# Kernel optimization log

Hardware: AMD Instinct MI355X
Metric: run time of the kernel (lower is better)

Reference implementation:

```python
import jax, jax.numpy as jnp
import numpy as np

WL = 140        # window_length
TD_NUM = 14     # TimeDelayEnd - TimeDelaySta = 21 - 7
OFC = 119       # window_length - TimeDelayEnd
E1 = 119        # td_attn embed dim
E2 = 16         # cm_attn embed dim


def _mha(q, k, v, in_w, in_b, out_w, out_b):
    # single-head MultiheadAttention, torch convention: y = x @ W.T + b
    E = q.shape[-1]
    qp = q @ in_w[:E].T + in_b[:E]
    kp = k @ in_w[E:2 * E].T + in_b[E:2 * E]
    vp = v @ in_w[2 * E:].T + in_b[2 * E:]
    attn = jax.nn.softmax((qp * (E ** -0.5)) @ kp.T, axis=-1)
    return (attn @ vp) @ out_w.T + out_b


def setup_inputs() -> dict:
    key = jax.random.key(0)
    ks = jax.random.split(key, 24)
    n = lambda i, s: jax.random.normal(ks[i], s, dtype=jnp.float32) * 0.05
    return {
        "x": jax.random.normal(ks[0], (1, 1, 18, WL), dtype=jnp.float32),
        "td_in_w": n(1, (3 * E1, E1)), "td_in_b": n(2, (3 * E1,)),
        "td_out_w": n(3, (E1, E1)), "td_out_b": n(4, (E1,)),
        "cm_in_w": n(5, (4, 3 * E2, E2)), "cm_in_b": n(6, (4, 3 * E2)),
        "cm_out_w": n(7, (4, E2, E2)), "cm_out_b": n(8, (4, E2)),
        "mc_w": n(9, (2, 16)), "mc_b": n(10, (2,)),
        "max_fc_w": n(11, (16, 32)), "max_fc_b": n(12, (16,)),
        "proj_w": n(13, (2, 16)),
        "ln_g": jnp.ones((16,), jnp.float32), "ln_b": jnp.zeros((16,), jnp.float32),
        "fc_w": n(14, (2,)), "fc_b": n(15, (2,)),
        "out1_w": n(16, (OFC, 2 * OFC)), "out1_b": n(17, (OFC,)),
        "out2_w": n(18, (2, OFC)), "out2_b": n(19, (2,)),
    }


def reference(x, td_in_w, td_in_b, td_out_w, td_out_b,
              cm_in_w, cm_in_b, cm_out_w, cm_out_b,
              mc_w, mc_b, max_fc_w, max_fc_b, proj_w,
              ln_g, ln_b, fc_w, fc_b, out1_w, out1_b, out2_w, out2_b):
    wavA = x[0, 0, 0]            # [140]
    eeg = x[0, 0, 1:17]          # [16, 140]
    wavB = x[0, 0, 17]           # [140]

    # ChannelWav: vectorized sliding-window gather -> [OFC, TD_NUM]
    idx = jnp.arange(OFC)[:, None] + jnp.arange(TD_NUM)[None, :]
    wA_win = wavA[idx]           # [119, 14]
    wB_win = wavB[idx]

    eeg_q = eeg[:, WL - OFC:]    # [16, 119] (16 eeg channels as seq, embed=119)

    # time-delay attention: query=eeg (len 16), key/value=delayed wav (len 14)
    wA_att = _mha(eeg_q, wA_win.T, wA_win.T, td_in_w, td_in_b, td_out_w, td_out_b)  # [16,119]
    wB_att = _mha(eeg_q, wB_win.T, wB_win.T, td_in_w, td_in_b, td_out_w, td_out_b)

    # select_max: bmm + 1x1 conv + relu + fc + argmax over 16 scores
    vA = jax.nn.relu(mc_w[0] @ (eeg_q @ wA_att.T) + mc_b[0])   # [16]
    vB = jax.nn.relu(mc_w[1] @ (eeg_q @ wB_att.T) + mc_b[1])
    weight = jax.nn.relu(max_fc_w @ jnp.concatenate([vA, vB]) + max_fc_b)
    mi = jnp.argmax(weight)     # note: clamped into [0, TD_NUM) by jnp.take
    wA_sel = jnp.take(wA_win.T, mi, axis=0)   # [119]
    wB_sel = jnp.take(wB_win.T, mi, axis=0)

    # proj_audio: Conv1d(1,16,1,bias=False) == outer product with weight vector
    wA_p = proj_w[0][:, None] * wA_sel[None, :]   # [16,119]
    wB_p = proj_w[1][:, None] * wB_sel[None, :]

    # LayerNorm over the 16-channel axis
    et = eeg_q.T                                   # [119,16]
    mu = et.mean(-1, keepdims=True)
    var = et.var(-1, keepdims=True)
    eeg_ln = (((et - mu) / jnp.sqrt(var + 1e-5)) * ln_g + ln_b).T   # [16,119]

    data = [wA_p, eeg_ln, eeg_ln, wB_p]
    kv = [eeg_ln, wA_p, wB_p, eeg_ln]
    outs = [_mha(data[i].T, kv[i].T, kv[i].T,
                 cm_in_w[i], cm_in_b[i], cm_out_w[i], cm_out_b[i]).T
            for i in range(4)]                      # each [16,119]

    # tensordot + diag == per-position channel dot product
    d0 = jnp.einsum('ct,ct->t', outs[0], outs[1])   # [119]
    d1 = jnp.einsum('ct,ct->t', outs[3], outs[2])
    s0 = jax.nn.sigmoid(fc_w[0] * d0 + fc_b[0])
    s1 = jax.nn.sigmoid(fc_w[1] * d1 + fc_b[1])
    dd = jnp.concatenate([s0, s1])                  # [238]

    h = jax.nn.sigmoid(out1_w @ dd + out1_b)
    return jax.nn.sigmoid(out2_w @ h + out2_b)[None, :]   # [1,2]
```

## Files before the change

### kernel.cpp

```cpp
#include <hip/hip_runtime.h>
#include <math.h>


#define NWG 8
#define NT  1024

constexpr int WLEN = 140;
constexpr int TDN  = 14;
constexpr int NOFC = 119;

constexpr int G_V16 = 0;
constexpr int G_DD  = 64;

constexpr int EEG = 0;
constexpr int WA  = 1904;
constexpr int WB  = 2044;
constexpr int LNT = 2184;
constexpr int QP4 = 4088;
constexpr int Z4  = 4564;
constexpr int UD  = 5040;
constexpr int WTT = 5160;
constexpr int WVV = 5280;
constexpr int VT  = 5400;
constexpr int SC4 = 5416;
constexpr int BKQ = 5472;
constexpr int CVB = 5476, CBO = 5477;
constexpr int WQH = 5480;
constexpr int WKL = 5496;
constexpr int WVL = 5512;
constexpr int WQT = 5528;
constexpr int CST = 5544;
constexpr int AC  = 5548;
constexpr int BC  = 5564;
constexpr int G1L = 5580;
constexpr int MXT = 5612;
constexpr int MXB = 6124;
constexpr int KPH = 6144;
constexpr int VPS = 8048;
constexpr int S1H = 10428;
constexpr int S2H = 10547;
constexpr int OWS = 10668;
constexpr int OBS = 10924;
constexpr int O1W = 10944;
constexpr int O1B = 14544;
constexpr int O2WS= 14560;
constexpr int O2B = 14590;
constexpr int FCW = 14592;
constexpr int FCB = 14594;
constexpr int DDL = 14596;
constexpr int HHL = 14836;
constexpr int VSL = 14852;
constexpr int ARENA = 14884;

struct Args {
  const float *x, *td_in_w, *td_in_b, *td_out_w, *td_out_b;
  const float *cm_in_w, *cm_in_b, *cm_out_w, *cm_out_b;
  const float *mc_w, *mc_b, *max_fc_w, *max_fc_b, *proj_w;
  const float *ln_g, *ln_b, *fc_w, *fc_b;
  const float *out1_w, *out1_b, *out2_w, *out2_b;
  float *out;
  unsigned int *bar;
  float *G;
};

__device__ __forceinline__ float sigmf(float v) {
  return 1.0f / (1.0f + __expf(-v));
}

__device__ __forceinline__ void gbar(unsigned int* p) {
  __syncthreads();
  if (threadIdx.x == 0) {
    __hip_atomic_fetch_add(p, 1u, __ATOMIC_ACQ_REL, __HIP_MEMORY_SCOPE_AGENT);
    while (__hip_atomic_load(p, __ATOMIC_RELAXED, __HIP_MEMORY_SCOPE_AGENT) < (unsigned)NWG) {
      __builtin_amdgcn_s_sleep(1);
    }
    __builtin_amdgcn_fence(__ATOMIC_ACQUIRE, "agent");
  }
  __syncthreads();
}

__device__ __forceinline__ float dot119(const float* __restrict__ w,
                                        const float* __restrict__ x,
                                        int lane16) {
  float a0 = 0.f, a1 = 0.f;
#pragma unroll
  for (int t = 0; t < 7; ++t) {
    float wv = w[lane16 + 16 * t];
    float xv = x[lane16 + 16 * t];
    if (t & 1) a1 += wv * xv; else a0 += wv * xv;
  }
  if (lane16 < 7) a0 += w[112 + lane16] * x[112 + lane16];
  float acc = a0 + a1;
#pragma unroll
  for (int m = 1; m < 16; m <<= 1) acc += __shfl_xor(acc, m);
  return acc;
}

__device__ __forceinline__ float dot16f4(const float* __restrict__ x,
                                         const float* __restrict__ w) {
  const float4* xa = (const float4*)x; const float4* wa = (const float4*)w;
  float4 x0 = xa[0], x1 = xa[1], x2 = xa[2], x3 = xa[3];
  float4 w0 = wa[0], w1 = wa[1], w2 = wa[2], w3 = wa[3];
  float d0 = x0.x*w0.x + x0.y*w0.y + x0.z*w0.z + x0.w*w0.w;
  float d1 = x1.x*w1.x + x1.y*w1.y + x1.z*w1.z + x1.w*w1.w;
  float d2 = x2.x*w2.x + x2.y*w2.y + x2.z*w2.z + x2.w*w2.w;
  float d3 = x3.x*w3.x + x3.y*w3.y + x3.z*w3.z + x3.w*w3.w;
  return (d0 + d1) + (d2 + d3);
}

__global__ __launch_bounds__(NT) void fused_cnn_kernel(Args a) {
  __shared__ __align__(16) float S[ARENA];
  const int tid = threadIdx.x;
  const int wgid = blockIdx.x;
  const int grp = tid >> 4;
  const int lane16 = tid & 15;
  float* G = a.G;

  const int s  = wgid >> 2;
  const int i0 = (wgid & 3) * 4;
  const int mh = s ? 3 : 0;
  const int lm = s ? 2 : 1;
  const int q4 = wgid & 3;
  const int r0 = q4 * 30;
  const int nr = (q4 == 3) ? 29 : 30;
  const int wavX = s ? WB : WA;

  for (int t = tid; t < 16 * NOFC; t += NT) {
    int c = t / NOFC, tt = t - c * NOFC;
    S[EEG + t] = a.x[(1 + c) * WLEN + (WLEN - NOFC) + tt];
  }
  if (tid < WLEN) {
    S[WA + tid] = a.x[tid];
    S[WB + tid] = a.x[17 * WLEN + tid];
  }
  if (tid < 512) {
    int t16 = tid >> 5, c32 = tid & 31;
    S[MXT + c32 * 16 + t16] = a.max_fc_w[tid];
  }
  if (tid < 16)  S[MXB + tid] = a.max_fc_b[tid];
  for (int idx = tid; idx < 15 * 238; idx += NT) {
    int rl = idx / 238, c = idx - rl * 238;
    int r = wgid * 15 + rl;
    S[O1W + rl * 240 + c] = (r < NOFC) ? a.out1_w[r * 238 + c] : 0.0f;
  }
  if (tid < 15) {
    int r = wgid * 15 + tid;
    S[O1B + tid] = (r < NOFC) ? a.out1_b[r] : 0.0f;
  }
  if (tid < 30) {
    int o = tid / 15, j = tid - o * 15;
    int r = wgid * 15 + j;
    S[O2WS + tid] = (r < NOFC) ? a.out2_w[o * NOFC + r] : 0.0f;
  }
  if (tid < 2) {
    S[O2B + tid] = a.out2_b[tid];
    S[FCW + tid] = a.fc_w[tid];
    S[FCB + tid] = a.fc_b[tid];
  }
  __syncthreads();

  for (int e = grp; e < NOFC; e += 64) {
    const float* wrow = a.td_in_w + e * NOFC;
    float w0 = wrow[lane16], w1 = wrow[lane16 + 16], w2 = wrow[lane16 + 32],
          w3 = wrow[lane16 + 48], w4 = wrow[lane16 + 64], w5 = wrow[lane16 + 80],
          w6 = wrow[lane16 + 96];
    float wt7 = (lane16 < 7) ? wrow[112 + lane16] : 0.0f;
    float b = a.td_in_b[e];
#pragma unroll
    for (int kk = 0; kk < 4; ++kk) {
      const float* x = S + EEG + (i0 + kk) * NOFC;
      float acc = w0 * x[lane16] + w1 * x[lane16 + 16] + w2 * x[lane16 + 32]
                + w3 * x[lane16 + 48] + w4 * x[lane16 + 64] + w5 * x[lane16 + 80]
                + w6 * x[lane16 + 96];
      if (lane16 < 7) acc += wt7 * x[112 + lane16];
#pragma unroll
      for (int mm = 1; mm < 16; mm <<= 1) acc += __shfl_xor(acc, mm);
      if (lane16 == 0) S[QP4 + kk * NOFC + e] = acc + b;
    }
  }
  if (grp >= 55) {
    int d = (grp - 55) * 16 + lane16;
    if (d < NOFC) {
      float acc = 0.f;
#pragma unroll
      for (int i = 0; i < 16; ++i) acc += a.mc_w[s * 16 + i] * S[EEG + i * NOFC + d];
      S[UD + d] = acc;
    }
  }
  __syncthreads();

  if (tid < NOFC) {
    float xv[16]; float mu = 0.f;
#pragma unroll
    for (int c = 0; c < 16; ++c) { xv[c] = S[EEG + c * NOFC + tid]; mu += xv[c]; }
    mu *= (1.0f / 16.0f);
    float var = 0.f;
#pragma unroll
    for (int c = 0; c < 16; ++c) { float d = xv[c] - mu; var += d * d; }
    var *= (1.0f / 16.0f);
    float inv = 1.0f / sqrtf(var + 1e-5f);
#pragma unroll
    for (int c = 0; c < 16; ++c)
      S[LNT + tid * 16 + c] = (xv[c] - mu) * inv * a.ln_g[c] + a.ln_b[c];
  } else if (tid >= 128 && tid < 128 + NOFC) {
    int t = tid - 128;
    float a0 = 0.f, a1 = 0.f, a2 = 0.f, a3 = 0.f;
    for (int e = 0; e < NOFC; ++e) {
      float w = a.td_in_w[(NOFC + e) * NOFC + t];
      a0 += S[QP4 + e] * w;
      a1 += S[QP4 + NOFC + e] * w;
      a2 += S[QP4 + 2 * NOFC + e] * w;
      a3 += S[QP4 + 3 * NOFC + e] * w;
    }
    S[Z4 + t] = a0; S[Z4 + NOFC + t] = a1;
    S[Z4 + 2 * NOFC + t] = a2; S[Z4 + 3 * NOFC + t] = a3;
  } else if (tid >= 256 && tid < 320) {
    int kk = (tid - 256) >> 4;
    float acc = dot119(S + QP4 + kk * NOFC, a.td_in_b + NOFC, lane16);
    if (lane16 == 0) S[BKQ + kk] = acc;
  } else if (tid >= 320 && tid < 320 + NOFC) {
    int t = tid - 320;
    float acc = 0.f;
    for (int d = 0; d < NOFC; ++d) acc += S[UD + d] * a.td_out_w[d * NOFC + t];
    S[WTT + t] = acc;
  } else if (tid >= 448 && tid < 464) {
    int e = tid - 448;
    float acc = 0.f;
#pragma unroll
    for (int c = 0; c < 16; ++c) acc += a.proj_w[s * 16 + c] * a.cm_in_w[(mh * 48 + e) * 16 + c];
    S[WQH + e] = acc;
  } else if (tid >= 464 && tid < 480) {
    int e = tid - 464;
    float acc = 0.f;
#pragma unroll
    for (int c = 0; c < 16; ++c) acc += a.proj_w[s * 16 + c] * a.cm_in_w[(lm * 48 + 16 + e) * 16 + c];
    S[WKL + e] = acc;
  } else if (tid >= 480 && tid < 496) {
    int e = tid - 480;
    float acc = 0.f;
#pragma unroll
    for (int c = 0; c < 16; ++c) acc += a.proj_w[s * 16 + c] * a.cm_in_w[(lm * 48 + 32 + e) * 16 + c];
    S[WVL + e] = acc;
  }
  if (grp >= 36) {
#pragma unroll
    for (int rnd = 0; rnd < 2; ++rnd) {
      int idx = (grp - 36) + rnd * 28;
      if (idx < 56) {
        int kk = idx / TDN, j = idx - kk * TDN;
        float acc = dot119(S + wavX + j, S + Z4 + kk * NOFC, lane16);
        if (lane16 == 0)
          S[SC4 + kk * TDN + j] = 0.09166984970282113f * (acc + S[BKQ + kk]);
      }
    }
  }
  __syncthreads();

  if (tid < NOFC) {
    float acc = 0.f;
    for (int e = 0; e < NOFC; ++e) acc += S[WTT + e] * a.td_in_w[(2 * NOFC + e) * NOFC + tid];
    S[WVV + tid] = acc;
  } else if (tid >= 120 && tid < 124) {
    int k = tid - 120;
    float* r = S + SC4 + k * TDN;
    float mx = r[0];
#pragma unroll
    for (int j = 1; j < TDN; ++j) mx = fmaxf(mx, r[j]);
    float sum = 0.f;
#pragma unroll
    for (int j = 0; j < TDN; ++j) { float p = __expf(r[j] - mx); r[j] = p; sum += p; }
    float inv = 1.0f / sum;
#pragma unroll
    for (int j = 0; j < TDN; ++j) r[j] *= inv;
  } else if (tid >= 128 && tid < 144) {
    int c = tid - 128;
    float acc = 0.f;
#pragma unroll
    for (int e = 0; e < 16; ++e) acc += a.cm_in_w[(lm * 48 + e) * 16 + c] * S[WKL + e];
    S[WQT + c] = acc;
  } else if (tid == 144) {
    float acc = 0.f;
#pragma unroll
    for (int e = 0; e < 16; ++e) acc += a.cm_in_b[lm * 48 + e] * S[WKL + e];
    S[CST] = acc;
  } else if (tid >= 160 && tid < 176) {
    int c = tid - 160;
    float acc = 0.f;
#pragma unroll
    for (int e = 0; e < 16; ++e) acc += a.cm_out_w[lm * 256 + c * 16 + e] * S[WVL + e];
    S[AC + c] = acc;
  } else if (tid >= 176 && tid < 192) {
    int c = tid - 176;
    float acc = 0.f;
#pragma unroll
    for (int e = 0; e < 16; ++e) acc += a.cm_out_w[lm * 256 + c * 16 + e] * a.cm_in_b[lm * 48 + 32 + e];
    S[BC + c] = acc + a.cm_out_b[lm * 16 + c];
  } else if (tid == 192) {
    float acc = 0.f;
    for (int e = 0; e < NOFC; ++e) acc += a.td_in_b[2 * NOFC + e] * S[WTT + e];
    S[CVB] = acc;
  } else if (tid == 193) {
    float acc = 0.f;
    for (int d = 0; d < NOFC; ++d) acc += S[UD + d] * a.td_out_b[d];
    S[CBO] = acc;
  }
  if (tid >= 256) {
    for (int o = tid - 256; o < 4080; o += 768) {
      if (o < 1904) {
        int u = o >> 4, e = o & 15;
        S[KPH + o] = dot16f4(S + LNT + u * 16, a.cm_in_w + (mh * 48 + 16 + e) * 16)
                     + a.cm_in_b[mh * 48 + 16 + e];
      } else if (o < 3808) {
        int o2 = o - 1904, u = o2 >> 4, e = o2 & 15;
        S[VPS + u * 20 + e] = dot16f4(S + LNT + u * 16, a.cm_in_w + (mh * 48 + 32 + e) * 16)
                              + a.cm_in_b[mh * 48 + 32 + e];
      } else if (o < 4064) {
        int o2 = o - 3808, c = o2 >> 4, e = o2 & 15;
        S[OWS + e * 16 + c] = a.cm_out_w[mh * 256 + o2];
      } else {
        S[OBS + o - 4064] = a.cm_out_b[mh * 16 + (o - 4064)];
      }
    }
  }
  __syncthreads();

  if (grp < TDN) {
    float acc = dot119(S + wavX + grp, S + WVV, lane16);
    if (lane16 == 0) S[VT + grp] = acc;
  }
  if (tid >= 256 && tid < 256 + 30) {
    int rl = tid - 256;
    if (rl < nr) {
      int t = r0 + rl;
      float acc = S[CST];
#pragma unroll
      for (int c = 0; c < 16; ++c) acc += S[LNT + t * 16 + c] * S[WQT + c];
      S[G1L + rl] = acc;
    }
  }
  if (tid >= 512 && tid < 512 + 238) {
    int idx = tid - 512;
    int u = (idx < NOFC) ? idx : idx - NOFC;
    const float* kpr = S + KPH + u * 16;
    float acc = 0.f;
    if (idx < NOFC) {
#pragma unroll
      for (int e = 0; e < 16; ++e) acc += S[WQH + e] * kpr[e];
      S[S1H + u] = acc;
    } else {
#pragma unroll
      for (int e = 0; e < 16; ++e) acc += a.cm_in_b[mh * 48 + e] * kpr[e];
      S[S2H + u] = acc;
    }
  }
  __syncthreads();

  if (tid < 4) {
    float acc = 0.f;
#pragma unroll
    for (int j = 0; j < TDN; ++j) acc += S[SC4 + tid * TDN + j] * S[VT + j];
    float v = acc + S[CVB] + S[CBO] + a.mc_b[s];
    G[G_V16 + s * 16 + i0 + tid] = fmaxf(v, 0.f);
  }
  gbar(a.bar + 0);

  if (tid < 32) S[VSL + tid] = G[G_V16 + tid];
  __syncthreads();
  int mi;
  {
    float wl = S[MXB + lane16];
#pragma unroll
    for (int c = 0; c < 32; ++c) wl += S[MXT + c * 16 + lane16] * S[VSL + c];
    wl = fmaxf(wl, 0.f);
    float mx = wl;
#pragma unroll
    for (int d = 1; d < 16; d <<= 1) mx = fmaxf(mx, __shfl_xor(mx, d));
    int cand = (wl == mx) ? lane16 : 99;
#pragma unroll
    for (int d = 1; d < 16; d <<= 1) cand = min(cand, __shfl_xor(cand, d));
    mi = min(cand, TDN - 1);
  }

  if (grp < nr) {
    const int t = r0 + grp;
    const float wselq = S[wavX + t + mi];
    float p[8];
    float sum = 0.f;
#pragma unroll
    for (int cc = 0; cc < 8; ++cc) {
      int u = lane16 + cc * 16;
      float e1 = 0.f;
      if (u < NOFC)
        e1 = __expf(0.25f * (wselq * S[S1H + u] + S[S2H + u]));
      p[cc] = e1;
      sum += e1;
    }
#pragma unroll
    for (int d = 1; d < 16; d <<= 1) sum += __shfl_xor(sum, d);
    float inv = 1.0f / sum;

    float oa[16];
#pragma unroll
    for (int e = 0; e < 16; ++e) oa[e] = 0.f;
#pragma unroll
    for (int cc = 0; cc < 8; ++cc) {
      int u = lane16 + cc * 16;
      if (u < NOFC) {
        const float4* v4 = (const float4*)(S + VPS + u * 20);
        float4 v0 = v4[0], v1 = v4[1], v2 = v4[2], v3 = v4[3];
        float pv = p[cc];
        oa[0] += pv*v0.x; oa[1] += pv*v0.y; oa[2] += pv*v0.z; oa[3] += pv*v0.w;
        oa[4] += pv*v1.x; oa[5] += pv*v1.y; oa[6] += pv*v1.z; oa[7] += pv*v1.w;
        oa[8] += pv*v2.x; oa[9] += pv*v2.y; oa[10] += pv*v2.z; oa[11] += pv*v2.w;
        oa[12] += pv*v3.x; oa[13] += pv*v3.y; oa[14] += pv*v3.z; oa[15] += pv*v3.w;
      }
    }
#pragma unroll
    for (int e = 0; e < 16; ++e) {
#pragma unroll
      for (int d = 1; d < 16; d <<= 1) oa[e] += __shfl_xor(oa[e], d);
    }
    float oc = S[OBS + lane16];
#pragma unroll
    for (int e = 0; e < 16; ++e) oc += oa[e] * inv * S[OWS + e * 16 + lane16];
    float dA = oc * S[AC + lane16];
    float dB = oc * S[BC + lane16];
#pragma unroll
    for (int d = 1; d < 16; d <<= 1) {
      dA += __shfl_xor(dA, d);
      dB += __shfl_xor(dB, d);
    }
    const float g = S[G1L + grp];
    float s0 = 0.f, s1a = 0.f;
#pragma unroll
    for (int cc = 0; cc < 8; ++cc) {
      int u = lane16 + cc * 16;
      if (u < NOFC) {
        float w = S[wavX + u + mi];
        float e1 = __expf(0.25f * g * w);
        s0 += e1; s1a += e1 * w;
      }
    }
#pragma unroll
    for (int d = 1; d < 16; d <<= 1) {
      s0 += __shfl_xor(s0, d);
      s1a += __shfl_xor(s1a, d);
    }
    float h = s1a / s0;
    float dval = h * dA + dB;
    if (lane16 == 0)
      G[G_DD + s * NOFC + t] = sigmf(S[FCW + s] * dval + S[FCB + s]);
  }
  gbar(a.bar + 16);

  if (tid < 238) S[DDL + tid] = G[G_DD + tid];
  __syncthreads();
  if (grp < 15) {
    int r = wgid * 15 + grp;
    float acc = 0.f;
#pragma unroll
    for (int k = 0; k < 15; ++k) {
      int c = lane16 + 16 * k;
      if (c < 238) acc += S[O1W + grp * 240 + c] * S[DDL + c];
    }
#pragma unroll
    for (int d = 1; d < 16; d <<= 1) acc += __shfl_xor(acc, d);
    if (lane16 == 0)
      S[HHL + grp] = (r < NOFC) ? sigmf(acc + S[O1B + grp]) : 0.0f;
  }
  __syncthreads();
  if (tid == 0) {
    float p0 = 0.f, p1 = 0.f;
#pragma unroll
    for (int j = 0; j < 15; ++j) {
      p0 += S[O2WS + j] * S[HHL + j];
      p1 += S[O2WS + 15 + j] * S[HHL + j];
    }
    float* acc = (float*)((char*)a.bar + 128);
    unsigned int* done = (unsigned int*)((char*)a.bar + 192);
    __hip_atomic_fetch_add(acc + 0, p0, __ATOMIC_RELAXED, __HIP_MEMORY_SCOPE_AGENT);
    __hip_atomic_fetch_add(acc + 1, p1, __ATOMIC_RELAXED, __HIP_MEMORY_SCOPE_AGENT);
    unsigned old = __hip_atomic_fetch_add(done, 1u, __ATOMIC_ACQ_REL, __HIP_MEMORY_SCOPE_AGENT);
    if (old == NWG - 1) {
      __builtin_amdgcn_fence(__ATOMIC_ACQUIRE, "agent");
      float a0 = __hip_atomic_load(acc + 0, __ATOMIC_RELAXED, __HIP_MEMORY_SCOPE_AGENT);
      float a1 = __hip_atomic_load(acc + 1, __ATOMIC_RELAXED, __HIP_MEMORY_SCOPE_AGENT);
      a.out[0] = sigmf(a0 + S[O2B + 0]);
      a.out[1] = sigmf(a1 + S[O2B + 1]);
    }
  }
}

extern "C" void kernel_launch(void* const* d_in, const int* in_sizes, int n_in,
                              void* d_out, int out_size, void* d_ws, size_t ws_size,
                              hipStream_t stream) {
  Args a;
  a.x        = (const float*)d_in[0];
  a.td_in_w  = (const float*)d_in[1];
  a.td_in_b  = (const float*)d_in[2];
  a.td_out_w = (const float*)d_in[3];
  a.td_out_b = (const float*)d_in[4];
  a.cm_in_w  = (const float*)d_in[5];
  a.cm_in_b  = (const float*)d_in[6];
  a.cm_out_w = (const float*)d_in[7];
  a.cm_out_b = (const float*)d_in[8];
  a.mc_w     = (const float*)d_in[9];
  a.mc_b     = (const float*)d_in[10];
  a.max_fc_w = (const float*)d_in[11];
  a.max_fc_b = (const float*)d_in[12];
  a.proj_w   = (const float*)d_in[13];
  a.ln_g     = (const float*)d_in[14];
  a.ln_b     = (const float*)d_in[15];
  a.fc_w     = (const float*)d_in[16];
  a.fc_b     = (const float*)d_in[17];
  a.out1_w   = (const float*)d_in[18];
  a.out1_b   = (const float*)d_in[19];
  a.out2_w   = (const float*)d_in[20];
  a.out2_b   = (const float*)d_in[21];
  a.out      = (float*)d_out;
  a.bar      = (unsigned int*)d_ws;
  a.G        = (float*)((char*)d_ws + 512);

  hipMemsetAsync(d_ws, 0, 512, stream);
  fused_cnn_kernel<<<dim3(NWG), dim3(NT), 0, stream>>>(a);
}
```

Baseline: 34.66 us.

## Remove final grid barrier via atomic partial out1 sums and split-K td matvecs

```diff
diff --git a/kernel.cpp b/kernel.cpp
--- a/kernel.cpp
+++ b/kernel.cpp
@@ -10,47 +10,47 @@
 constexpr int NOFC = 119;
 
 constexpr int G_V16 = 0;
-constexpr int G_DD  = 64;
 
 constexpr int EEG = 0;
 constexpr int WA  = 1904;
 constexpr int WB  = 2044;
 constexpr int LNT = 2184;
 constexpr int QP4 = 4088;
-constexpr int Z4  = 4564;
-constexpr int UD  = 5040;
-constexpr int WTT = 5160;
-constexpr int WVV = 5280;
-constexpr int VT  = 5400;
-constexpr int SC4 = 5416;
-constexpr int BKQ = 5472;
-constexpr int CVB = 5476, CBO = 5477;
-constexpr int WQH = 5480;
-constexpr int WKL = 5496;
-constexpr int WVL = 5512;
-constexpr int WQT = 5528;
-constexpr int CST = 5544;
-constexpr int AC  = 5548;
-constexpr int BC  = 5564;
-constexpr int G1L = 5580;
-constexpr int MXT = 5612;
-constexpr int MXB = 6124;
-constexpr int KPH = 6144;
-constexpr int VPS = 8048;
-constexpr int S1H = 10428;
-constexpr int S2H = 10547;
-constexpr int OWS = 10668;
-constexpr int OBS = 10924;
-constexpr int O1W = 10944;
-constexpr int O1B = 14544;
-constexpr int O2WS= 14560;
-constexpr int O2B = 14590;
-constexpr int FCW = 14592;
-constexpr int FCB = 14594;
-constexpr int DDL = 14596;
-constexpr int HHL = 14836;
-constexpr int VSL = 14852;
-constexpr int ARENA = 14884;
+constexpr int Z8  = 4564;
+constexpr int UD  = 5516;
+constexpr int WT2 = 5636;
+constexpr int WV2 = 5876;
+constexpr int VT  = 6114;
+constexpr int SC4 = 6128;
+constexpr int BKQ = 6184;
+constexpr int CVB = 6188, CBO = 6189;
+constexpr int WQH = 6192;
+constexpr int WKL = 6208;
+constexpr int WVL = 6224;
+constexpr int WQT = 6240;
+constexpr int CST = 6256;
+constexpr int AC  = 6260;
+constexpr int BC  = 6276;
+constexpr int G1L = 6292;
+constexpr int MXT = 6324;
+constexpr int MXB = 6836;
+constexpr int KPH = 6852;
+constexpr int VPS = 8756;
+constexpr int S1H = 11136;
+constexpr int S2H = 11255;
+constexpr int OWS = 11376;
+constexpr int OBS = 11632;
+constexpr int O1C = 11648;
+constexpr int O1B = 15340;
+constexpr int O2WS= 15460;
+constexpr int O2B = 15698;
+constexpr int FCW = 15700;
+constexpr int FCB = 15702;
+constexpr int DD30= 15704;
+constexpr int HH  = 15736;
+constexpr int VSL = 15856;
+constexpr int FLG = 15888;
+constexpr int ARENA = 15892;
 
 struct Args {
   const float *x, *td_in_w, *td_in_b, *td_out_w, *td_out_b;
@@ -138,20 +138,17 @@
     S[MXT + c32 * 16 + t16] = a.max_fc_w[tid];
   }
   if (tid < 16)  S[MXB + tid] = a.max_fc_b[tid];
-  for (int idx = tid; idx < 15 * 238; idx += NT) {
-    int rl = idx / 238, c = idx - rl * 238;
-    int r = wgid * 15 + rl;
-    S[O1W + rl * 240 + c] = (r < NOFC) ? a.out1_w[r * 238 + c] : 0.0f;
-  }
-  if (tid < 15) {
-    int r = wgid * 15 + tid;
-    S[O1B + tid] = (r < NOFC) ? a.out1_b[r] : 0.0f;
-  }
-  if (tid < 30) {
-    int o = tid / 15, j = tid - o * 15;
-    int r = wgid * 15 + j;
-    S[O2WS + tid] = (r < NOFC) ? a.out2_w[o * NOFC + r] : 0.0f;
-  }
+  if (tid < 256) {
+    int c = tid >> 4, e = tid & 15;
+    S[OWS + e * 16 + c] = a.cm_out_w[mh * 256 + tid];
+  }
+  if (tid < 16)  S[OBS + tid] = a.cm_out_b[mh * 16 + tid];
+  for (int idx = tid; idx < 119 * 30; idx += NT) {
+    int r = idx / 30, j = idx - r * 30;
+    if (j < nr) S[O1C + r * 31 + j] = a.out1_w[r * 238 + s * NOFC + r0 + j];
+  }
+  if (tid < NOFC) S[O1B + tid] = a.out1_b[tid];
+  if (tid < 238)  S[O2WS + tid] = a.out2_w[tid];
   if (tid < 2) {
     S[O2B + tid] = a.out2_b[tid];
     S[FCW + tid] = a.fc_w[tid];
@@ -202,45 +199,71 @@
 #pragma unroll
     for (int c = 0; c < 16; ++c)
       S[LNT + tid * 16 + c] = (xv[c] - mu) * inv * a.ln_g[c] + a.ln_b[c];
-  } else if (tid >= 128 && tid < 128 + NOFC) {
-    int t = tid - 128;
+  } else if (tid >= 128 && tid < 366) {
+    int i = tid - 128, half = i / NOFC, t = i - half * NOFC;
+    int e0 = half * 60, e1 = half ? NOFC : 60;
     float a0 = 0.f, a1 = 0.f, a2 = 0.f, a3 = 0.f;
-    for (int e = 0; e < NOFC; ++e) {
+    for (int e = e0; e < e1; ++e) {
       float w = a.td_in_w[(NOFC + e) * NOFC + t];
       a0 += S[QP4 + e] * w;
       a1 += S[QP4 + NOFC + e] * w;
       a2 += S[QP4 + 2 * NOFC + e] * w;
       a3 += S[QP4 + 3 * NOFC + e] * w;
     }
-    S[Z4 + t] = a0; S[Z4 + NOFC + t] = a1;
-    S[Z4 + 2 * NOFC + t] = a2; S[Z4 + 3 * NOFC + t] = a3;
-  } else if (tid >= 256 && tid < 320) {
-    int kk = (tid - 256) >> 4;
+    S[Z8 + (half * 4 + 0) * NOFC + t] = a0;
+    S[Z8 + (half * 4 + 1) * NOFC + t] = a1;
+    S[Z8 + (half * 4 + 2) * NOFC + t] = a2;
+    S[Z8 + (half * 4 + 3) * NOFC + t] = a3;
+  } else if (tid >= 384 && tid < 448) {
+    int kk = (tid - 384) >> 4;
     float acc = dot119(S + QP4 + kk * NOFC, a.td_in_b + NOFC, lane16);
     if (lane16 == 0) S[BKQ + kk] = acc;
-  } else if (tid >= 320 && tid < 320 + NOFC) {
-    int t = tid - 320;
-    float acc = 0.f;
-    for (int d = 0; d < NOFC; ++d) acc += S[UD + d] * a.td_out_w[d * NOFC + t];
-    S[WTT + t] = acc;
-  } else if (tid >= 448 && tid < 464) {
-    int e = tid - 448;
+  } else if (tid >= 448 && tid < 686) {
+    int i = tid - 448, half = i / NOFC, t = i - half * NOFC;
+    int d0 = half * 60, d1 = half ? NOFC : 60;
+    float acc = 0.f;
+    for (int d = d0; d < d1; ++d) acc += S[UD + d] * a.td_out_w[d * NOFC + t];
+    S[WT2 + half * NOFC + t] = acc;
+  } else if (tid >= 704 && tid < 720) {
+    int e = tid - 704;
     float acc = 0.f;
 #pragma unroll
     for (int c = 0; c < 16; ++c) acc += a.proj_w[s * 16 + c] * a.cm_in_w[(mh * 48 + e) * 16 + c];
     S[WQH + e] = acc;
-  } else if (tid >= 464 && tid < 480) {
-    int e = tid - 464;
+  } else if (tid >= 720 && tid < 736) {
+    int e = tid - 720;
     float acc = 0.f;
 #pragma unroll
     for (int c = 0; c < 16; ++c) acc += a.proj_w[s * 16 + c] * a.cm_in_w[(lm * 48 + 16 + e) * 16 + c];
     S[WKL + e] = acc;
-  } else if (tid >= 480 && tid < 496) {
-    int e = tid - 480;
+  } else if (tid >= 736 && tid < 752) {
+    int e = tid - 736;
     float acc = 0.f;
 #pragma unroll
     for (int c = 0; c < 16; ++c) acc += a.proj_w[s * 16 + c] * a.cm_in_w[(lm * 48 + 32 + e) * 16 + c];
     S[WVL + e] = acc;
+  }
+  __syncthreads();
+
+  if (tid < 238) {
+    int half = tid / NOFC, t = tid - half * NOFC;
+    int e0 = half * 60, e1 = half ? NOFC : 60;
+    float acc = 0.f;
+    for (int e = e0; e < e1; ++e)
+      acc += (S[WT2 + e] + S[WT2 + NOFC + e]) * a.td_in_w[(2 * NOFC + e) * NOFC + t];
+    S[WV2 + half * NOFC + t] = acc;
+  } else if (tid >= 240 && tid < 560) {
+    for (int o = tid - 240; o < 3808; o += 320) {
+      if (o < 1904) {
+        int u = o >> 4, e = o & 15;
+        S[KPH + o] = dot16f4(S + LNT + u * 16, a.cm_in_w + (mh * 48 + 16 + e) * 16)
+                     + a.cm_in_b[mh * 48 + 16 + e];
+      } else {
+        int o2 = o - 1904, u = o2 >> 4, e = o2 & 15;
+        S[VPS + u * 20 + e] = dot16f4(S + LNT + u * 16, a.cm_in_w + (mh * 48 + 32 + e) * 16)
+                              + a.cm_in_b[mh * 48 + 32 + e];
+      }
+    }
   }
   if (grp >= 36) {
 #pragma unroll
@@ -248,7 +271,8 @@
       int idx = (grp - 36) + rnd * 28;
       if (idx < 56) {
         int kk = idx / TDN, j = idx - kk * TDN;
-        float acc = dot119(S + wavX + j, S + Z4 + kk * NOFC, lane16);
+        float acc = dot119(S + wavX + j, S + Z8 + kk * NOFC, lane16)
+                  + dot119(S + wavX + j, S + Z8 + (4 + kk) * NOFC, lane16);
         if (lane16 == 0)
           S[SC4 + kk * TDN + j] = 0.09166984970282113f * (acc + S[BKQ + kk]);
       }
@@ -256,12 +280,12 @@
   }
   __syncthreads();
 
-  if (tid < NOFC) {
-    float acc = 0.f;
-    for (int e = 0; e < NOFC; ++e) acc += S[WTT + e] * a.td_in_w[(2 * NOFC + e) * NOFC + tid];
-    S[WVV + tid] = acc;
-  } else if (tid >= 120 && tid < 124) {
-    int k = tid - 120;
+  if (grp < TDN) {
+    float acc = dot119(S + wavX + grp, S + WV2, lane16)
+              + dot119(S + wavX + grp, S + WV2 + NOFC, lane16);
+    if (lane16 == 0) S[VT + grp] = acc;
+  } else if (tid >= 224 && tid < 228) {
+    int k = tid - 224;
     float* r = S + SC4 + k * TDN;
     float mx = r[0];
 #pragma unroll
@@ -272,64 +296,62 @@
     float inv = 1.0f / sum;
 #pragma unroll
     for (int j = 0; j < TDN; ++j) r[j] *= inv;
-  } else if (tid >= 128 && tid < 144) {
-    int c = tid - 128;
+  } else if (grp == 15) {
+    float acc = dot119(a.td_in_b + 2 * NOFC, S + WT2, lane16)
+              + dot119(a.td_in_b + 2 * NOFC, S + WT2 + NOFC, lane16);
+    if (lane16 == 0) S[CVB] = acc;
+  } else if (grp == 16) {
+    float acc = dot119(S + UD, a.td_out_b, lane16);
+    if (lane16 == 0) S[CBO] = acc;
+  } else if (tid >= 288 && tid < 304) {
+    int c = tid - 288;
     float acc = 0.f;
 #pragma unroll
     for (int e = 0; e < 16; ++e) acc += a.cm_in_w[(lm * 48 + e) * 16 + c] * S[WKL + e];
     S[WQT + c] = acc;
-  } else if (tid == 144) {
+  } else if (tid == 304) {
     float acc = 0.f;
 #pragma unroll
     for (int e = 0; e < 16; ++e) acc += a.cm_in_b[lm * 48 + e] * S[WKL + e];
     S[CST] = acc;
-  } else if (tid >= 160 && tid < 176) {
-    int c = tid - 160;
+  } else if (tid >= 320 && tid < 336) {
+    int c = tid - 320;
     float acc = 0.f;
 #pragma unroll
     for (int e = 0; e < 16; ++e) acc += a.cm_out_w[lm * 256 + c * 16 + e] * S[WVL + e];
     S[AC + c] = acc;
-  } else if (tid >= 176 && tid < 192) {
-    int c = tid - 176;
+  } else if (tid >= 336 && tid < 352) {
+    int c = tid - 336;
     float acc = 0.f;
 #pragma unroll
     for (int e = 0; e < 16; ++e) acc += a.cm_out_w[lm * 256 + c * 16 + e] * a.cm_in_b[lm * 48 + 32 + e];
     S[BC + c] = acc + a.cm_out_b[lm * 16 + c];
-  } else if (tid == 192) {
-    float acc = 0.f;
-    for (int e = 0; e < NOFC; ++e) acc += a.td_in_b[2 * NOFC + e] * S[WTT + e];
-    S[CVB] = acc;
-  } else if (tid == 193) {
-    float acc = 0.f;
-    for (int d = 0; d < NOFC; ++d) acc += S[UD + d] * a.td_out_b[d];
-    S[CBO] = acc;
-  }
-  if (tid >= 256) {
-    for (int o = tid - 256; o < 4080; o += 768) {
-      if (o < 1904) {
-        int u = o >> 4, e = o & 15;
-        S[KPH + o] = dot16f4(S + LNT + u * 16, a.cm_in_w + (mh * 48 + 16 + e) * 16)
-                     + a.cm_in_b[mh * 48 + 16 + e];
-      } else if (o < 3808) {
-        int o2 = o - 1904, u = o2 >> 4, e = o2 & 15;
-        S[VPS + u * 20 + e] = dot16f4(S + LNT + u * 16, a.cm_in_w + (mh * 48 + 32 + e) * 16)
-                              + a.cm_in_b[mh * 48 + 32 + e];
-      } else if (o < 4064) {
-        int o2 = o - 3808, c = o2 >> 4, e = o2 & 15;
-        S[OWS + e * 16 + c] = a.cm_out_w[mh * 256 + o2];
-      } else {
-        S[OBS + o - 4064] = a.cm_out_b[mh * 16 + (o - 4064)];
-      }
-    }
-  }
-  __syncthreads();
-
-  if (grp < TDN) {
-    float acc = dot119(S + wavX + grp, S + WVV, lane16);
-    if (lane16 == 0) S[VT + grp] = acc;
-  }
-  if (tid >= 256 && tid < 256 + 30) {
-    int rl = tid - 256;
+  }
+  if (tid >= 512 && tid < 750) {
+    int idx = tid - 512;
+    int u = (idx < NOFC) ? idx : idx - NOFC;
+    const float* kpr = S + KPH + u * 16;
+    float acc = 0.f;
+    if (idx < NOFC) {
+#pragma unroll
+      for (int e = 0; e < 16; ++e) acc += S[WQH + e] * kpr[e];
+      S[S1H + u] = acc;
+    } else {
+#pragma unroll
+      for (int e = 0; e < 16; ++e) acc += a.cm_in_b[mh * 48 + e] * kpr[e];
+      S[S2H + u] = acc;
+    }
+  }
+  __syncthreads();
+
+  if (tid < 4) {
+    float acc = 0.f;
+#pragma unroll
+    for (int j = 0; j < TDN; ++j) acc += S[SC4 + tid * TDN + j] * S[VT + j];
+    float v = acc + S[CVB] + S[CBO] + a.mc_b[s];
+    G[G_V16 + s * 16 + i0 + tid] = fmaxf(v, 0.f);
+  } else if (tid >= 32 && tid < 62) {
+    int rl = tid - 32;
     if (rl < nr) {
       int t = r0 + rl;
       float acc = S[CST];
@@ -337,30 +359,6 @@
       for (int c = 0; c < 16; ++c) acc += S[LNT + t * 16 + c] * S[WQT + c];
       S[G1L + rl] = acc;
     }
-  }
-  if (tid >= 512 && tid < 512 + 238) {
-    int idx = tid - 512;
-    int u = (idx < NOFC) ? idx : idx - NOFC;
-    const float* kpr = S + KPH + u * 16;
-    float acc = 0.f;
-    if (idx < NOFC) {
-#pragma unroll
-      for (int e = 0; e < 16; ++e) acc += S[WQH + e] * kpr[e];
-      S[S1H + u] = acc;
-    } else {
-#pragma unroll
-      for (int e = 0; e < 16; ++e) acc += a.cm_in_b[mh * 48 + e] * kpr[e];
-      S[S2H + u] = acc;
-    }
-  }
-  __syncthreads();
-
-  if (tid < 4) {
-    float acc = 0.f;
-#pragma unroll
-    for (int j = 0; j < TDN; ++j) acc += S[SC4 + tid * TDN + j] * S[VT + j];
-    float v = acc + S[CVB] + S[CBO] + a.mc_b[s];
-    G[G_V16 + s * 16 + i0 + tid] = fmaxf(v, 0.f);
   }
   gbar(a.bar + 0);
 
@@ -449,45 +447,42 @@
     float h = s1a / s0;
     float dval = h * dA + dB;
     if (lane16 == 0)
-      G[G_DD + s * NOFC + t] = sigmf(S[FCW + s] * dval + S[FCB + s]);
-  }
-  gbar(a.bar + 16);
-
-  if (tid < 238) S[DDL + tid] = G[G_DD + tid];
-  __syncthreads();
-  if (grp < 15) {
-    int r = wgid * 15 + grp;
-    float acc = 0.f;
-#pragma unroll
-    for (int k = 0; k < 15; ++k) {
-      int c = lane16 + 16 * k;
-      if (c < 238) acc += S[O1W + grp * 240 + c] * S[DDL + c];
-    }
-#pragma unroll
-    for (int d = 1; d < 16; d <<= 1) acc += __shfl_xor(acc, d);
-    if (lane16 == 0)
-      S[HHL + grp] = (r < NOFC) ? sigmf(acc + S[O1B + grp]) : 0.0f;
-  }
-  __syncthreads();
+      S[DD30 + grp] = sigmf(S[FCW + s] * dval + S[FCB + s]);
+  }
+  __syncthreads();
+
+  float* accG = (float*)((char*)a.bar + 128);
+  if (tid < NOFC) {
+    float acc = 0.f;
+    for (int j = 0; j < nr; ++j) acc += S[O1C + tid * 31 + j] * S[DD30 + j];
+    atomicAdd(accG + tid, acc);
+  }
+  __syncthreads();
+
+  unsigned int* done = (unsigned int*)((char*)a.bar + 640);
   if (tid == 0) {
-    float p0 = 0.f, p1 = 0.f;
-#pragma unroll
-    for (int j = 0; j < 15; ++j) {
-      p0 += S[O2WS + j] * S[HHL + j];
-      p1 += S[O2WS + 15 + j] * S[HHL + j];
-    }
-    float* acc = (float*)((char*)a.bar + 128);
-    unsigned int* done = (unsigned int*)((char*)a.bar + 192);
-    __hip_atomic_fetch_add(acc + 0, p0, __ATOMIC_RELAXED, __HIP_MEMORY_SCOPE_AGENT);
-    __hip_atomic_fetch_add(acc + 1, p1, __ATOMIC_RELAXED, __HIP_MEMORY_SCOPE_AGENT);
     unsigned old = __hip_atomic_fetch_add(done, 1u, __ATOMIC_ACQ_REL, __HIP_MEMORY_SCOPE_AGENT);
-    if (old == NWG - 1) {
-      __builtin_amdgcn_fence(__ATOMIC_ACQUIRE, "agent");
-      float a0 = __hip_atomic_load(acc + 0, __ATOMIC_RELAXED, __HIP_MEMORY_SCOPE_AGENT);
-      float a1 = __hip_atomic_load(acc + 1, __ATOMIC_RELAXED, __HIP_MEMORY_SCOPE_AGENT);
-      a.out[0] = sigmf(a0 + S[O2B + 0]);
-      a.out[1] = sigmf(a1 + S[O2B + 1]);
-    }
+    S[FLG] = (old == NWG - 1) ? 1.0f : 0.0f;
+  }
+  __syncthreads();
+  const bool last = (S[FLG] != 0.0f);
+  if (last && tid < NOFC) {
+    __builtin_amdgcn_fence(__ATOMIC_ACQUIRE, "agent");
+    S[HH + tid] = sigmf(accG[tid] + S[O1B + tid]);
+  }
+  __syncthreads();
+  if (last && tid < 32) {
+    int o2 = tid >> 4;
+    float a0 = 0.f;
+#pragma unroll
+    for (int t = 0; t < 8; ++t) {
+      int idx = lane16 + 16 * t;
+      if (idx < NOFC) a0 += S[O2WS + o2 * NOFC + idx] * S[HH + idx];
+    }
+    float acc = a0;
+#pragma unroll
+    for (int mm = 1; mm < 16; mm <<= 1) acc += __shfl_xor(acc, mm);
+    if (lane16 == 0) a.out[o2] = sigmf(acc + S[O2B + o2]);
   }
 }
 
@@ -519,8 +514,8 @@
   a.out2_b   = (const float*)d_in[21];
   a.out      = (float*)d_out;
   a.bar      = (unsigned int*)d_ws;
-  a.G        = (float*)((char*)d_ws + 512);
-
-  hipMemsetAsync(d_ws, 0, 512, stream);
+  a.G        = (float*)((char*)d_ws + 1024);
+
+  hipMemsetAsync(d_ws, 0, 1024, stream);
   fused_cnn_kernel<<<dim3(NWG), dim3(NT), 0, stream>>>(a);
 }
```

New measurement: 41.66 us. 20.2% more time.

## Rebalance pre-barrier phases so serial GEMV chains run in fewer synchronized stages

Applied to the files above, without the earlier changes.

```diff
diff --git a/kernel.cpp b/kernel.cpp
--- a/kernel.cpp
+++ b/kernel.cpp
@@ -48,8 +48,8 @@
 constexpr int FCW = 14592;
 constexpr int FCB = 14594;
 constexpr int DDL = 14596;
-constexpr int HHL = 14836;
-constexpr int VSL = 14852;
+constexpr int HHL = 14834;
+constexpr int VSL = 14850;
 constexpr int ARENA = 14884;
 
 struct Args {
@@ -138,6 +138,11 @@
     S[MXT + c32 * 16 + t16] = a.max_fc_w[tid];
   }
   if (tid < 16)  S[MXB + tid] = a.max_fc_b[tid];
+  if (tid < 256) {
+    int c = tid >> 4, e = tid & 15;
+    S[OWS + e * 16 + c] = a.cm_out_w[mh * 256 + tid];
+  }
+  if (tid < 16)  S[OBS + tid] = a.cm_out_b[mh * 16 + tid];
   for (int idx = tid; idx < 15 * 238; idx += NT) {
     int rl = idx / 238, c = idx - rl * 238;
     int r = wgid * 15 + rl;
@@ -190,39 +195,41 @@
   __syncthreads();
 
   if (tid < NOFC) {
-    float xv[16]; float mu = 0.f;
-#pragma unroll
-    for (int c = 0; c < 16; ++c) { xv[c] = S[EEG + c * NOFC + tid]; mu += xv[c]; }
-    mu *= (1.0f / 16.0f);
-    float var = 0.f;
-#pragma unroll
-    for (int c = 0; c < 16; ++c) { float d = xv[c] - mu; var += d * d; }
-    var *= (1.0f / 16.0f);
-    float inv = 1.0f / sqrtf(var + 1e-5f);
-#pragma unroll
-    for (int c = 0; c < 16; ++c)
-      S[LNT + tid * 16 + c] = (xv[c] - mu) * inv * a.ln_g[c] + a.ln_b[c];
-  } else if (tid >= 128 && tid < 128 + NOFC) {
-    int t = tid - 128;
     float a0 = 0.f, a1 = 0.f, a2 = 0.f, a3 = 0.f;
+    const float* base = a.td_in_w + NOFC * NOFC + tid;
     for (int e = 0; e < NOFC; ++e) {
-      float w = a.td_in_w[(NOFC + e) * NOFC + t];
+      float w = base[e * NOFC];
       a0 += S[QP4 + e] * w;
       a1 += S[QP4 + NOFC + e] * w;
       a2 += S[QP4 + 2 * NOFC + e] * w;
       a3 += S[QP4 + 3 * NOFC + e] * w;
     }
-    S[Z4 + t] = a0; S[Z4 + NOFC + t] = a1;
-    S[Z4 + 2 * NOFC + t] = a2; S[Z4 + 3 * NOFC + t] = a3;
-  } else if (tid >= 256 && tid < 320) {
-    int kk = (tid - 256) >> 4;
+    S[Z4 + tid] = a0; S[Z4 + NOFC + tid] = a1;
+    S[Z4 + 2 * NOFC + tid] = a2; S[Z4 + 3 * NOFC + tid] = a3;
+  } else if (tid >= 128 && tid < 128 + NOFC) {
+    int t = tid - 128;
+    float acc = 0.f;
+    const float* base = a.td_out_w + t;
+    for (int d = 0; d < NOFC; ++d) acc += S[UD + d] * base[d * NOFC];
+    S[WTT + t] = acc;
+  } else if (tid >= 256 && tid < 256 + NOFC) {
+    int t = tid - 256;
+    float xv[16]; float mu = 0.f;
+#pragma unroll
+    for (int c = 0; c < 16; ++c) { xv[c] = S[EEG + c * NOFC + t]; mu += xv[c]; }
+    mu *= (1.0f / 16.0f);
+    float var = 0.f;
+#pragma unroll
+    for (int c = 0; c < 16; ++c) { float d = xv[c] - mu; var += d * d; }
+    var *= (1.0f / 16.0f);
+    float inv = 1.0f / sqrtf(var + 1e-5f);
+#pragma unroll
+    for (int c = 0; c < 16; ++c)
+      S[LNT + t * 16 + c] = (xv[c] - mu) * inv * a.ln_g[c] + a.ln_b[c];
+  } else if (tid >= 384 && tid < 448) {
+    int kk = (tid - 384) >> 4;
     float acc = dot119(S + QP4 + kk * NOFC, a.td_in_b + NOFC, lane16);
     if (lane16 == 0) S[BKQ + kk] = acc;
-  } else if (tid >= 320 && tid < 320 + NOFC) {
-    int t = tid - 320;
-    float acc = 0.f;
-    for (int d = 0; d < NOFC; ++d) acc += S[UD + d] * a.td_out_w[d * NOFC + t];
-    S[WTT + t] = acc;
   } else if (tid >= 448 && tid < 464) {
     int e = tid - 448;
     float acc = 0.f;
@@ -241,6 +248,26 @@
 #pragma unroll
     for (int c = 0; c < 16; ++c) acc += a.proj_w[s * 16 + c] * a.cm_in_w[(lm * 48 + 32 + e) * 16 + c];
     S[WVL + e] = acc;
+  }
+  __syncthreads();
+
+  if (tid < NOFC) {
+    float acc = 0.f;
+    const float* base = a.td_in_w + 2 * NOFC * NOFC + tid;
+    for (int e = 0; e < NOFC; ++e) acc += S[WTT + e] * base[e * NOFC];
+    S[WVV + tid] = acc;
+  } else if (tid >= 128 && tid < 560) {
+    for (int o = tid - 128; o < 3808; o += 432) {
+      if (o < 1904) {
+        int u = o >> 4, e = o & 15;
+        S[KPH + o] = dot16f4(S + LNT + u * 16, a.cm_in_w + (mh * 48 + 16 + e) * 16)
+                     + a.cm_in_b[mh * 48 + 16 + e];
+      } else {
+        int o2 = o - 1904, u = o2 >> 4, e = o2 & 15;
+        S[VPS + u * 20 + e] = dot16f4(S + LNT + u * 16, a.cm_in_w + (mh * 48 + 32 + e) * 16)
+                              + a.cm_in_b[mh * 48 + 32 + e];
+      }
+    }
   }
   if (grp >= 36) {
 #pragma unroll
@@ -256,80 +283,76 @@
   }
   __syncthreads();
 
-  if (tid < NOFC) {
-    float acc = 0.f;
-    for (int e = 0; e < NOFC; ++e) acc += S[WTT + e] * a.td_in_w[(2 * NOFC + e) * NOFC + tid];
-    S[WVV + tid] = acc;
-  } else if (tid >= 120 && tid < 124) {
-    int k = tid - 120;
-    float* r = S + SC4 + k * TDN;
-    float mx = r[0];
-#pragma unroll
-    for (int j = 1; j < TDN; ++j) mx = fmaxf(mx, r[j]);
-    float sum = 0.f;
-#pragma unroll
-    for (int j = 0; j < TDN; ++j) { float p = __expf(r[j] - mx); r[j] = p; sum += p; }
-    float inv = 1.0f / sum;
-#pragma unroll
-    for (int j = 0; j < TDN; ++j) r[j] *= inv;
-  } else if (tid >= 128 && tid < 144) {
-    int c = tid - 128;
-    float acc = 0.f;
-#pragma unroll
-    for (int e = 0; e < 16; ++e) acc += a.cm_in_w[(lm * 48 + e) * 16 + c] * S[WKL + e];
-    S[WQT + c] = acc;
-  } else if (tid == 144) {
-    float acc = 0.f;
-#pragma unroll
-    for (int e = 0; e < 16; ++e) acc += a.cm_in_b[lm * 48 + e] * S[WKL + e];
-    S[CST] = acc;
-  } else if (tid >= 160 && tid < 176) {
-    int c = tid - 160;
-    float acc = 0.f;
-#pragma unroll
-    for (int e = 0; e < 16; ++e) acc += a.cm_out_w[lm * 256 + c * 16 + e] * S[WVL + e];
-    S[AC + c] = acc;
-  } else if (tid >= 176 && tid < 192) {
-    int c = tid - 176;
-    float acc = 0.f;
-#pragma unroll
-    for (int e = 0; e < 16; ++e) acc += a.cm_out_w[lm * 256 + c * 16 + e] * a.cm_in_b[lm * 48 + 32 + e];
-    S[BC + c] = acc + a.cm_out_b[lm * 16 + c];
-  } else if (tid == 192) {
-    float acc = 0.f;
-    for (int e = 0; e < NOFC; ++e) acc += a.td_in_b[2 * NOFC + e] * S[WTT + e];
-    S[CVB] = acc;
-  } else if (tid == 193) {
-    float acc = 0.f;
-    for (int d = 0; d < NOFC; ++d) acc += S[UD + d] * a.td_out_b[d];
-    S[CBO] = acc;
-  }
-  if (tid >= 256) {
-    for (int o = tid - 256; o < 4080; o += 768) {
-      if (o < 1904) {
-        int u = o >> 4, e = o & 15;
-        S[KPH + o] = dot16f4(S + LNT + u * 16, a.cm_in_w + (mh * 48 + 16 + e) * 16)
-                     + a.cm_in_b[mh * 48 + 16 + e];
-      } else if (o < 3808) {
-        int o2 = o - 1904, u = o2 >> 4, e = o2 & 15;
-        S[VPS + u * 20 + e] = dot16f4(S + LNT + u * 16, a.cm_in_w + (mh * 48 + 32 + e) * 16)
-                              + a.cm_in_b[mh * 48 + 32 + e];
-      } else if (o < 4064) {
-        int o2 = o - 3808, c = o2 >> 4, e = o2 & 15;
-        S[OWS + e * 16 + c] = a.cm_out_w[mh * 256 + o2];
-      } else {
-        S[OBS + o - 4064] = a.cm_out_b[mh * 16 + (o - 4064)];
-      }
-    }
-  }
-  __syncthreads();
-
   if (grp < TDN) {
     float acc = dot119(S + wavX + grp, S + WVV, lane16);
     if (lane16 == 0) S[VT + grp] = acc;
-  }
-  if (tid >= 256 && tid < 256 + 30) {
-    int rl = tid - 256;
+  } else if (tid >= 224 && tid < 228) {
+    int k = tid - 224;
+    float* r = S + SC4 + k * TDN;
+    float mx = r[0];
+#pragma unroll
+    for (int j = 1; j < TDN; ++j) mx = fmaxf(mx, r[j]);
+    float sum = 0.f;
+#pragma unroll
+    for (int j = 0; j < TDN; ++j) { float p = __expf(r[j] - mx); r[j] = p; sum += p; }
+    float inv = 1.0f / sum;
+#pragma unroll
+    for (int j = 0; j < TDN; ++j) r[j] *= inv;
+  } else if (grp == 15) {
+    float acc = dot119(a.td_in_b + 2 * NOFC, S + WTT, lane16);
+    if (lane16 == 0) S[CVB] = acc;
+  } else if (grp == 16) {
+    float acc = dot119(S + UD, a.td_out_b, lane16);
+    if (lane16 == 0) S[CBO] = acc;
+  } else if (tid >= 288 && tid < 304) {
+    int c = tid - 288;
+    float acc = 0.f;
+#pragma unroll
+    for (int e = 0; e < 16; ++e) acc += a.cm_in_w[(lm * 48 + e) * 16 + c] * S[WKL + e];
+    S[WQT + c] = acc;
+  } else if (tid == 304) {
+    float acc = 0.f;
+#pragma unroll
+    for (int e = 0; e < 16; ++e) acc += a.cm_in_b[lm * 48 + e] * S[WKL + e];
+    S[CST] = acc;
+  } else if (tid >= 320 && tid < 336) {
+    int c = tid - 320;
+    float acc = 0.f;
+#pragma unroll
+    for (int e = 0; e < 16; ++e) acc += a.cm_out_w[lm * 256 + c * 16 + e] * S[WVL + e];
+    S[AC + c] = acc;
+  } else if (tid >= 336 && tid < 352) {
+    int c = tid - 336;
+    float acc = 0.f;
+#pragma unroll
+    for (int e = 0; e < 16; ++e) acc += a.cm_out_w[lm * 256 + c * 16 + e] * a.cm_in_b[lm * 48 + 32 + e];
+    S[BC + c] = acc + a.cm_out_b[lm * 16 + c];
+  }
+  if (tid >= 512 && tid < 750) {
+    int idx = tid - 512;
+    int u = (idx < NOFC) ? idx : idx - NOFC;
+    const float* kpr = S + KPH + u * 16;
+    float acc = 0.f;
+    if (idx < NOFC) {
+#pragma unroll
+      for (int e = 0; e < 16; ++e) acc += S[WQH + e] * kpr[e];
+      S[S1H + u] = acc;
+    } else {
+#pragma unroll
+      for (int e = 0; e < 16; ++e) acc += a.cm_in_b[mh * 48 + e] * kpr[e];
+      S[S2H + u] = acc;
+    }
+  }
+  __syncthreads();
+
+  if (tid < 4) {
+    float acc = 0.f;
+#pragma unroll
+    for (int j = 0; j < TDN; ++j) acc += S[SC4 + tid * TDN + j] * S[VT + j];
+    float v = acc + S[CVB] + S[CBO] + a.mc_b[s];
+    G[G_V16 + s * 16 + i0 + tid] = fmaxf(v, 0.f);
+  } else if (tid >= 32 && tid < 62) {
+    int rl = tid - 32;
     if (rl < nr) {
       int t = r0 + rl;
       float acc = S[CST];
@@ -337,30 +360,6 @@
       for (int c = 0; c < 16; ++c) acc += S[LNT + t * 16 + c] * S[WQT + c];
       S[G1L + rl] = acc;
     }
-  }
-  if (tid >= 512 && tid < 512 + 238) {
-    int idx = tid - 512;
-    int u = (idx < NOFC) ? idx : idx - NOFC;
-    const float* kpr = S + KPH + u * 16;
-    float acc = 0.f;
-    if (idx < NOFC) {
-#pragma unroll
-      for (int e = 0; e < 16; ++e) acc += S[WQH + e] * kpr[e];
-      S[S1H + u] = acc;
-    } else {
-#pragma unroll
-      for (int e = 0; e < 16; ++e) acc += a.cm_in_b[mh * 48 + e] * kpr[e];
-      S[S2H + u] = acc;
-    }
-  }
-  __syncthreads();
-
-  if (tid < 4) {
-    float acc = 0.f;
-#pragma unroll
-    for (int j = 0; j < TDN; ++j) acc += S[SC4 + tid * TDN + j] * S[VT + j];
-    float v = acc + S[CVB] + S[CBO] + a.mc_b[s];
-    G[G_V16 + s * 16 + i0 + tid] = fmaxf(v, 0.f);
   }
   gbar(a.bar + 0);
 
```

After: 35.20 us. No clear change (+1.5%).
